# Kernel tuning notes

Hardware: AMD Instinct MI355X
Metric: run time of the kernel (lower is better)

The kernel has to match this reference:

```python
import jax, jax.numpy as jnp
import numpy as np

B, C, H, W = 32, 256, 32, 32
HID = 64


def setup_inputs() -> dict:
    key = jax.random.key(0)
    k1, k2, k3, k4, k5, k6 = jax.random.split(key, 6)
    query_features = jax.random.normal(k1, (B, C, H, W), dtype=jnp.float32)
    key_features = jax.random.normal(k2, (B, C, H, W), dtype=jnp.float32)
    # 1x1 conv weights == per-pixel linear maps [out_c, in_c] + bias
    s = 1.0 / np.sqrt(C)
    Wq = jax.random.uniform(k3, (HID, C), jnp.float32, -s, s)
    bq = jax.random.uniform(k4, (HID,), jnp.float32, -s, s)
    Wk = jax.random.uniform(k5, (HID, C), jnp.float32, -s, s)
    bk = jax.random.uniform(k6, (HID,), jnp.float32, -s, s)
    return {"query_features": query_features, "key_features": key_features,
            "Wq": Wq, "bq": bq, "Wk": Wk, "bk": bk,
            "vis_CA": 0, "same_WqWk": 0}


def reference(query_features, key_features, Wq, bq, Wk, bk, vis_CA, same_WqWk):
    b, c, h, w = query_features.shape
    # 1x1 conv projections (bias broadcast over spatial dims)
    Q = jnp.einsum('bchw,oc->bohw', query_features, Wq) + bq[None, :, None, None]
    if same_WqWk:
        K = jnp.einsum('bchw,oc->bohw', key_features, Wq) + bq[None, :, None, None]
    else:
        K = jnp.einsum('bchw,oc->bohw', key_features, Wk) + bk[None, :, None, None]
    V = key_features.reshape(b, c, h * w)              # b c (h w)
    # unscaled dense spatial attention: [b, h, w, h*w]
    attn = jnp.einsum('bcij,bckl->bijkl', Q, K).reshape(b, h, w, h * w)
    attn = jax.nn.softmax(attn, axis=3)
    attended = jnp.einsum('bijp,bcp->bcij', attn, V)   # [b, c, h, w]
    return attended
```

## Files before the change

kernel.cpp:

```cpp
#include <hip/hip_runtime.h>

typedef __bf16 bf16;
typedef __attribute__((ext_vector_type(4))) __bf16 bf16x4;
typedef __attribute__((ext_vector_type(8))) __bf16 bf16x8;
typedef __attribute__((ext_vector_type(4))) float f32x4;
typedef unsigned int u32;

#define MFMA16(a, b, c) __builtin_amdgcn_mfma_f32_16x16x32_bf16((a), (b), (c), 0, 0, 0)
#define LOG2E 1.4426950408889634f
#define AS1 __attribute__((address_space(1)))
#define AS3 __attribute__((address_space(3)))
#define GLL16(g, l) __builtin_amdgcn_global_load_lds((const AS1 u32*)(g), (AS3 u32*)(l), 16, 0, 0)


__global__ __launch_bounds__(256) void wprep_kernel(const float* __restrict__ Wq,
                                                    const float* __restrict__ Wk,
                                                    const int* __restrict__ flag,
                                                    bf16* __restrict__ Wbh,
                                                    bf16* __restrict__ Wbl) {
  const int bx = blockIdx.x, t = threadIdx.x;
  int z = bx >> 4;
  const float* src = (z == 0) ? Wq : ((flag[0] != 0) ? Wq : Wk);
  const float sc = (z == 0) ? LOG2E : 1.0f;
  int i = ((((bx & 15) << 8) + t) << 2);
  float4 vv = *(const float4*)(src + i);
  vv.x *= sc; vv.y *= sc; vv.z *= sc; vv.w *= sc;
  bf16x4 hi, lo;
  hi[0] = (bf16)vv.x; lo[0] = (bf16)(vv.x - (float)hi[0]);
  hi[1] = (bf16)vv.y; lo[1] = (bf16)(vv.y - (float)hi[1]);
  hi[2] = (bf16)vv.z; lo[2] = (bf16)(vv.z - (float)hi[2]);
  hi[3] = (bf16)vv.w; lo[3] = (bf16)(vv.w - (float)hi[3]);
  *(bf16x4*)(Wbh + (z << 14) + i) = hi;
  *(bf16x4*)(Wbl + (z << 14) + i) = lo;
}

__global__ __launch_bounds__(256) void prep_kernel(const float* __restrict__ qf,
                                                   const float* __restrict__ kf,
                                                   const bf16* __restrict__ Wbh,
                                                   const bf16* __restrict__ Wbl,
                                                   const float* __restrict__ bq,
                                                   const float* __restrict__ bk,
                                                   const int* __restrict__ flag,
                                                   bf16* __restrict__ Qp,
                                                   bf16* __restrict__ KV) {
  const int bid = blockIdx.x, t = threadIdx.x;
  if (bid >= 512) {
    int i = ((bid - 512) << 8) + t;
    int q8 = i & 127, c = (i >> 7) & 255, b = i >> 15;
    const float* src = kf + ((size_t)(((b << 8) + c)) << 10) + (q8 << 3);
    float4 f0 = *(const float4*)src;
    float4 f1 = *(const float4*)(src + 4);
    bf16x8 v;
    v[0] = (bf16)f0.x; v[1] = (bf16)f0.y; v[2] = (bf16)f0.z; v[3] = (bf16)f0.w;
    v[4] = (bf16)f1.x; v[5] = (bf16)f1.y; v[6] = (bf16)f1.z; v[7] = (bf16)f1.w;
    int kt = q8 >> 4, mm = q8 & 15;
    char* dst = (char*)KV + (size_t)((b << 3) + kt) * 81920 + 16384 +
                ((c >> 6) << 14) + ((mm >> 2) << 12) + (((c >> 4) & 3) << 10) +
                ((mm & 3) << 8) + ((c & 15) << 4);
    *(bf16x8*)dst = v;
    return;
  }
  const int bx = bid;
  const int x = bx & 7, b = (bx >> 3) & 31, z = bx >> 8;
  const float* xg = z ? kf : qf;
  const bf16* Wh = Wbh + z * 16384;
  const bf16* Wl = Wbl + z * 16384;
  const float* bias = z ? (flag[0] ? bq : bk) : bq;

  const int w = t >> 6, lane = t & 63;
  const int g = lane >> 4, l16 = lane & 15;
  const int wo = w >> 1, wp = w & 1;
  const int o0 = wo << 5;
  const int pbase = (x << 7) + (wp << 6);

  f32x4 acc[2][4];
#pragma unroll
  for (int ot = 0; ot < 2; ++ot) {
    float4 bv = *(const float4*)(bias + o0 + (ot << 4) + (g << 2));
    if (z == 0) { bv.x *= LOG2E; bv.y *= LOG2E; bv.z *= LOG2E; bv.w *= LOG2E; }
#pragma unroll
    for (int pt = 0; pt < 4; ++pt) acc[ot][pt] = (f32x4){bv.x, bv.y, bv.z, bv.w};
  }

  const float* xb = xg + ((((b << 8) + (g << 3)) << 10) + pbase + l16);
  const bf16* whb = Wh + ((o0 + l16) << 8) + (g << 3);
  const bf16* wlb = Wl + ((o0 + l16) << 8) + (g << 3);

  for (int kk = 0; kk < 8; ++kk) {
    bf16x8 ah[2], al[2];
#pragma unroll
    for (int ot = 0; ot < 2; ++ot) {
      ah[ot] = *(const bf16x8*)(whb + (ot << 12) + (kk << 5));
      al[ot] = *(const bf16x8*)(wlb + (ot << 12) + (kk << 5));
    }
    const float* xk = xb + (kk << 15);
#pragma unroll
    for (int pt = 0; pt < 4; ++pt) {
      float xv[8];
#pragma unroll
      for (int j = 0; j < 8; ++j) xv[j] = xk[(j << 10) + (pt << 4)];
      bf16x8 xf;
#pragma unroll
      for (int j = 0; j < 8; ++j) xf[j] = (bf16)xv[j];
#pragma unroll
      for (int ot = 0; ot < 2; ++ot) {
        acc[ot][pt] = MFMA16(ah[ot], xf, acc[ot][pt]);
        acc[ot][pt] = MFMA16(al[ot], xf, acc[ot][pt]);
      }
    }
  }

#pragma unroll
  for (int ot = 0; ot < 2; ++ot)
#pragma unroll
    for (int pt = 0; pt < 4; ++pt) {
      bf16x4 q4;
#pragma unroll
      for (int r = 0; r < 4; ++r) q4[r] = (bf16)acc[ot][pt][r];
      int p = pbase + (pt << 4) + l16;
      if (z == 0) {
        *(bf16x4*)(Qp + ((((b << 10) + p)) << 6) + o0 + (ot << 4) + (g << 2)) = q4;
      } else {
        int kt = p >> 7, q = p & 127;
        int blk = (o0 >> 3) + (ot << 1) + (g >> 1);
        char* dst = (char*)KV + (size_t)((b << 3) + kt) * 81920 + q * 128 +
                    16 * (blk ^ (q & 7)) + ((g & 1) << 3);
        *(bf16x4*)dst = q4;
      }
    }
}

__global__ __launch_bounds__(256, 2) void attn_kernel(const bf16* __restrict__ KV,
                                                      const bf16* __restrict__ Qp,
                                                      float* __restrict__ out) {
  const int bid = blockIdx.x;
  const int wkid = ((bid & 7) << 6) + (bid >> 3);
  const int b = wkid >> 4, ptile = wkid & 15;
  const int p0 = ptile << 6;
  const int t = threadIdx.x;
  const int w = t >> 6, lane = t & 63;
  const int u = lane >> 4, l16 = lane & 15;

  __shared__ __align__(16) unsigned char sK[2][16384];
  __shared__ __align__(16) unsigned char sP[16384];
  __shared__ float sL[64];

  const bf16* qb = Qp + (((size_t)((b << 10) + p0 + (w << 4) + l16)) << 6) + (u << 3);
  const bf16x8 qa0 = *(const bf16x8*)qb;
  const bf16x8 qa1 = *(const bf16x8*)(qb + 32);

  const char* chunk0 = (const char*)KV + (size_t)b * (8 * 81920);
  const int Rb = ((l16 >> 2) << 3) + ((l16 & 3) << 1);

  f32x4 acc[4][4];
#pragma unroll
  for (int i = 0; i < 4; ++i)
#pragma unroll
    for (int j = 0; j < 4; ++j) acc[i][j] = (f32x4){0.f, 0.f, 0.f, 0.f};
  float l_ = 0.f;

  const int prow = (w << 4) + l16, pswz = prow & 7;

  {
    const char* g = chunk0 + (w << 12) + (lane << 4);
    unsigned char* l = sK[0] + (w << 12);
#pragma unroll
    for (int op = 0; op < 4; ++op) GLL16(g + op * 1024, l + op * 1024);
  }
  asm volatile("s_waitcnt vmcnt(0)" ::: "memory");
  __syncthreads();

  int cur = 0;
  for (int kt = 0; kt < 8; ++kt) {
    bf16x8 vr[16];
    const char* vsrc = chunk0 + kt * 81920 + 16384 + (w << 14) + (lane << 4);
#pragma unroll
    for (int k = 0; k < 16; ++k) vr[k] = *(const bf16x8*)(vsrc + (k << 10));
    if (kt < 7) {
      const char* g = chunk0 + (kt + 1) * 81920 + (w << 12) + (lane << 4);
      unsigned char* l = sK[cur ^ 1] + (w << 12);
#pragma unroll
      for (int op = 0; op < 4; ++op) GLL16(g + op * 1024, l + op * 1024);
    }
    const unsigned char* sKc = sK[cur];

    f32x4 s[8];
#pragma unroll
    for (int qt = 0; qt < 8; ++qt) {
      const int R = Rb + (qt & 1) + ((qt >> 1) << 5);
      const int rb = R * 128;
      bf16x8 k0 = *(const bf16x8*)(sKc + rb + 16 * (u ^ (R & 7)));
      bf16x8 k1 = *(const bf16x8*)(sKc + rb + 16 * ((u + 4) ^ (R & 7)));
      f32x4 z = (f32x4){0.f, 0.f, 0.f, 0.f};
      z = MFMA16(k0, qa0, z);
      s[qt] = MFMA16(k1, qa1, z);
    }
#pragma unroll
    for (int qt = 0; qt < 8; ++qt)
#pragma unroll
      for (int r = 0; r < 4; ++r) s[qt][r] = exp2f(s[qt][r]);
    float rs = 0.f;
#pragma unroll
    for (int qt = 0; qt < 8; ++qt)
      rs += (s[qt][0] + s[qt][1]) + (s[qt][2] + s[qt][3]);
    rs += __shfl_xor(rs, 16);
    rs += __shfl_xor(rs, 32);
    l_ += rs;
#pragma unroll
    for (int a = 0; a < 4; ++a) {
      bf16x8 pb;
#pragma unroll
      for (int r = 0; r < 4; ++r) {
        pb[2 * r] = (bf16)s[2 * a][r];
        pb[2 * r + 1] = (bf16)s[2 * a + 1][r];
      }
      *(bf16x8*)(sP + prow * 256 + 16 * (((a << 2) + u) ^ pswz)) = pb;
    }
    __syncthreads();

#pragma unroll
    for (int kb = 0; kb < 4; ++kb) {
      bf16x8 pbr[4];
#pragma unroll
      for (int pg = 0; pg < 4; ++pg) {
        const int rr = (pg << 4) + l16;
        pbr[pg] = *(const bf16x8*)(sP + rr * 256 + 16 * (((kb << 2) + u) ^ (rr & 7)));
      }
#pragma unroll
      for (int ct = 0; ct < 4; ++ct)
#pragma unroll
        for (int pg = 0; pg < 4; ++pg)
          acc[pg][ct] = MFMA16(vr[(kb << 2) + ct], pbr[pg], acc[pg][ct]);
    }
    asm volatile("s_waitcnt vmcnt(0)" ::: "memory");
    __syncthreads();
    cur ^= 1;
  }

  if (lane < 16) sL[(w << 4) + lane] = l_;
  __syncthreads();
#pragma unroll
  for (int pg = 0; pg < 4; ++pg) {
    const float inv = 1.f / sL[(pg << 4) + l16];
    float* ob = out + ((size_t)b << 18) + p0 + (pg << 4) + l16;
#pragma unroll
    for (int ct = 0; ct < 4; ++ct)
#pragma unroll
      for (int r = 0; r < 4; ++r) {
        int c = (w << 6) + (ct << 4) + (u << 2) + r;
        ob[(size_t)c << 10] = acc[pg][ct][r] * inv;
      }
  }
}

extern "C" void kernel_launch(void* const* d_in, const int* in_sizes, int n_in,
                              void* d_out, int out_size, void* d_ws, size_t ws_size,
                              hipStream_t stream) {
  const float* qf = (const float*)d_in[0];
  const float* kf = (const float*)d_in[1];
  const float* Wq = (const float*)d_in[2];
  const float* bq = (const float*)d_in[3];
  const float* Wk = (const float*)d_in[4];
  const float* bk = (const float*)d_in[5];
  const int* flag = (const int*)d_in[7];
  float* out = (float*)d_out;

  char* ws = (char*)d_ws;
  bf16* Qp = (bf16*)ws;
  bf16* Wbh = (bf16*)(ws + (4u << 20));
  bf16* Wbl = (bf16*)(ws + (4u << 20) + 65536);
  bf16* KV = (bf16*)(ws + (5u << 20));

  wprep_kernel<<<32, 256, 0, stream>>>(Wq, Wk, flag, Wbh, Wbl);
  prep_kernel<<<4608, 256, 0, stream>>>(qf, kf, Wbh, Wbl, bq, bk, flag, Qp, KV);
  attn_kernel<<<512, 256, 0, stream>>>(KV, Qp, out);
}
```

Before: 65.49 us.

## Fuse V bf16 conversion into projection kernel with LDS double-buffered input staging

```diff
diff --git a/kernel.cpp b/kernel.cpp
--- a/kernel.cpp
+++ b/kernel.cpp
@@ -44,24 +44,7 @@
                                                    bf16* __restrict__ Qp,
                                                    bf16* __restrict__ KV) {
   const int bid = blockIdx.x, t = threadIdx.x;
-  if (bid >= 512) {
-    int i = ((bid - 512) << 8) + t;
-    int q8 = i & 127, c = (i >> 7) & 255, b = i >> 15;
-    const float* src = kf + ((size_t)(((b << 8) + c)) << 10) + (q8 << 3);
-    float4 f0 = *(const float4*)src;
-    float4 f1 = *(const float4*)(src + 4);
-    bf16x8 v;
-    v[0] = (bf16)f0.x; v[1] = (bf16)f0.y; v[2] = (bf16)f0.z; v[3] = (bf16)f0.w;
-    v[4] = (bf16)f1.x; v[5] = (bf16)f1.y; v[6] = (bf16)f1.z; v[7] = (bf16)f1.w;
-    int kt = q8 >> 4, mm = q8 & 15;
-    char* dst = (char*)KV + (size_t)((b << 3) + kt) * 81920 + 16384 +
-                ((c >> 6) << 14) + ((mm >> 2) << 12) + (((c >> 4) & 3) << 10) +
-                ((mm & 3) << 8) + ((c & 15) << 4);
-    *(bf16x8*)dst = v;
-    return;
-  }
-  const int bx = bid;
-  const int x = bx & 7, b = (bx >> 3) & 31, z = bx >> 8;
+  const int x = bid & 7, b = (bid >> 3) & 31, z = bid >> 8;
   const float* xg = z ? kf : qf;
   const bf16* Wh = Wbh + z * 16384;
   const bf16* Wl = Wbl + z * 16384;
@@ -72,6 +55,13 @@
   const int wo = w >> 1, wp = w & 1;
   const int o0 = wo << 5;
   const int pbase = (x << 7) + (wp << 6);
+  const int qloc = (wp << 6) + l16;
+
+  __shared__ float sX[2][4160];
+
+  const int cl0 = t >> 4, oct = t & 15;
+  const float* srcb = xg + (((size_t)((b << 8) + cl0)) << 10) + (x << 7) + (oct << 3);
+  char* vdst0 = (char*)KV + (size_t)((b << 3) + x) * 81920 + 16384;
 
   f32x4 acc[2][4];
 #pragma unroll
@@ -82,32 +72,78 @@
     for (int pt = 0; pt < 4; ++pt) acc[ot][pt] = (f32x4){bv.x, bv.y, bv.z, bv.w};
   }
 
-  const float* xb = xg + ((((b << 8) + (g << 3)) << 10) + pbase + l16);
   const bf16* whb = Wh + ((o0 + l16) << 8) + (g << 3);
   const bf16* wlb = Wl + ((o0 + l16) << 8) + (g << 3);
 
+#pragma unroll
+  for (int it = 0; it < 2; ++it) {
+    const int cl = (it << 4) + cl0;
+    const float* s = srcb + ((size_t)it << 14);
+    float4 f0 = *(const float4*)s;
+    float4 f1 = *(const float4*)(s + 4);
+    float* d = &sX[0][cl * 130 + (oct << 3)];
+    *(float2*)(d + 0) = make_float2(f0.x, f0.y);
+    *(float2*)(d + 2) = make_float2(f0.z, f0.w);
+    *(float2*)(d + 4) = make_float2(f1.x, f1.y);
+    *(float2*)(d + 6) = make_float2(f1.z, f1.w);
+    if (z) {
+      int cg = cl;
+      bf16x8 v;
+      v[0] = (bf16)f0.x; v[1] = (bf16)f0.y; v[2] = (bf16)f0.z; v[3] = (bf16)f0.w;
+      v[4] = (bf16)f1.x; v[5] = (bf16)f1.y; v[6] = (bf16)f1.z; v[7] = (bf16)f1.w;
+      char* dst = vdst0 + ((cg >> 6) << 14) + ((oct >> 2) << 12) +
+                  (((cg >> 4) & 3) << 10) + ((oct & 3) << 8) + ((cg & 15) << 4);
+      *(bf16x8*)dst = v;
+    }
+  }
+  __syncthreads();
+
+#pragma unroll
   for (int kk = 0; kk < 8; ++kk) {
+    if (kk < 7) {
+      const int bi = (kk + 1) & 1;
+#pragma unroll
+      for (int it = 0; it < 2; ++it) {
+        const int cl = (it << 4) + cl0;
+        const float* s = srcb + ((size_t)it << 14) + ((size_t)(kk + 1) << 15);
+        float4 f0 = *(const float4*)s;
+        float4 f1 = *(const float4*)(s + 4);
+        float* d = &sX[bi][cl * 130 + (oct << 3)];
+        *(float2*)(d + 0) = make_float2(f0.x, f0.y);
+        *(float2*)(d + 2) = make_float2(f0.z, f0.w);
+        *(float2*)(d + 4) = make_float2(f1.x, f1.y);
+        *(float2*)(d + 6) = make_float2(f1.z, f1.w);
+        if (z) {
+          int cg = ((kk + 1) << 5) + cl;
+          bf16x8 v;
+          v[0] = (bf16)f0.x; v[1] = (bf16)f0.y; v[2] = (bf16)f0.z; v[3] = (bf16)f0.w;
+          v[4] = (bf16)f1.x; v[5] = (bf16)f1.y; v[6] = (bf16)f1.z; v[7] = (bf16)f1.w;
+          char* dst = vdst0 + ((cg >> 6) << 14) + ((oct >> 2) << 12) +
+                      (((cg >> 4) & 3) << 10) + ((oct & 3) << 8) + ((cg & 15) << 4);
+          *(bf16x8*)dst = v;
+        }
+      }
+    }
+    const float* sb = sX[kk & 1];
     bf16x8 ah[2], al[2];
 #pragma unroll
     for (int ot = 0; ot < 2; ++ot) {
       ah[ot] = *(const bf16x8*)(whb + (ot << 12) + (kk << 5));
       al[ot] = *(const bf16x8*)(wlb + (ot << 12) + (kk << 5));
     }
-    const float* xk = xb + (kk << 15);
 #pragma unroll
     for (int pt = 0; pt < 4; ++pt) {
-      float xv[8];
-#pragma unroll
-      for (int j = 0; j < 8; ++j) xv[j] = xk[(j << 10) + (pt << 4)];
       bf16x8 xf;
 #pragma unroll
-      for (int j = 0; j < 8; ++j) xf[j] = (bf16)xv[j];
+      for (int j = 0; j < 8; ++j)
+        xf[j] = (bf16)sb[(((g << 3) + j) * 130) + qloc + (pt << 4)];
 #pragma unroll
       for (int ot = 0; ot < 2; ++ot) {
         acc[ot][pt] = MFMA16(ah[ot], xf, acc[ot][pt]);
         acc[ot][pt] = MFMA16(al[ot], xf, acc[ot][pt]);
       }
     }
+    __syncthreads();
   }
 
 #pragma unroll
@@ -272,6 +308,6 @@
   bf16* KV = (bf16*)(ws + (5u << 20));
 
   wprep_kernel<<<32, 256, 0, stream>>>(Wq, Wk, flag, Wbh, Wbl);
-  prep_kernel<<<4608, 256, 0, stream>>>(qf, kf, Wbh, Wbl, bq, bk, flag, Qp, KV);
+  prep_kernel<<<512, 256, 0, stream>>>(qf, kf, Wbh, Wbl, bq, bk, flag, Qp, KV);
   attn_kernel<<<512, 256, 0, stream>>>(KV, Qp, out);
 }
```

After: 64.11 us. 2.1% less time.
